# Optimization experiments

Hardware: AMD Instinct MI355X
Metric: run time of the kernel (lower is better)

## Reference

```python
import jax, jax.numpy as jnp
import numpy as np

B = 16384      # samples
NN = 11        # causal-graph nodes per sample (adult)
D = 4          # per-node raw feature dim (node_dim_max)
F = 32         # dim_input_enc = h_dim_list_enc[0]
EDIM = 4       # edge_dim
NI = 3         # number of intervention features

_BASE_EDGES = np.array([[0,3],[0,4],[1,3],[1,5],[2,5],[0,6],[3,6],[4,7],[5,7],
                        [6,8],[7,8],[2,9],[8,9],[3,10],[6,10],[9,10],[1,10]], dtype=np.int64)


def setup_inputs() -> dict:
    key = jax.random.key(0)
    ks = jax.random.split(key, 14)
    # batched edge index: replicate the 17-edge DAG per sample with node offsets
    off = (np.arange(B) * NN)[:, None]                      # [B,1]
    src = (_BASE_EDGES[:, 0][None, :] + off).reshape(-1).astype(np.int32)  # [E]
    dst = (_BASE_EDGES[:, 1][None, :] + off).reshape(-1).astype(np.int32)
    E = src.shape[0]
    g = lambda k, shp, s: jax.random.normal(k, shp, dtype=jnp.float32) * s
    return {
        'x_input':  g(ks[0], (B, NN * D), 1.0),
        'edge_attr': g(ks[1], (E, EDIM), 1.0),
        'W_emb':   g(ks[2], (NN, D, F), 1.0 / np.sqrt(D)),
        'b_emb':   jnp.zeros((NN, F), jnp.float32),
        'W_pre1':  g(ks[3], (NI, 2 * F + EDIM, F), 1.0 / np.sqrt(2 * F + EDIM)),
        'b_pre1':  jnp.zeros((NI, F), jnp.float32),
        'W_post1': g(ks[4], (NI, 12 * F, F), 1.0 / np.sqrt(12 * F)),
        'b_post1': jnp.zeros((NI, F), jnp.float32),
        'W_pre2':  g(ks[5], (NI, 2 * F + EDIM, F), 1.0 / np.sqrt(2 * F + EDIM)),
        'b_pre2':  jnp.zeros((NI, F), jnp.float32),
        'W_post2': g(ks[6], (NI, 12 * F, 1), 1.0 / np.sqrt(12 * F)),
        'b_post2': jnp.zeros((NI, 1), jnp.float32),
        'W_fc':    g(ks[7], (NI, NN, 1), 1.0 / np.sqrt(NN)),
        'b_fc':    jnp.zeros((NI, 1), jnp.float32),
        'edge_src': jnp.asarray(src),
        'edge_dst': jnp.asarray(dst),
    }


def _pna_conv(h, src, dst, e, Wpre, bpre, Wpost, bpost, cnt_c, mask, amp, att, N):
    # message: pre-MLP over [h_dst, h_src, edge_attr]
    m = jax.nn.relu(jnp.concatenate([h[dst], h[src], e], axis=1) @ Wpre + bpre)  # [E,F]
    s = jax.ops.segment_sum(m, dst, num_segments=N)
    mean = s / cnt_c[:, None]
    mean_sq = jax.ops.segment_sum(m * m, dst, num_segments=N) / cnt_c[:, None]
    std = jnp.sqrt(jax.nn.relu(mean_sq - mean * mean) + 1e-5)
    mn = jnp.where(mask[:, None], jax.ops.segment_min(m, dst, num_segments=N), 0.0)
    mx = jnp.where(mask[:, None], jax.ops.segment_max(m, dst, num_segments=N), 0.0)
    agg = jnp.concatenate([mean, mn, mx, std], axis=1)                 # [N,4F]
    scaled = jnp.concatenate([agg, agg * amp[:, None], agg * att[:, None]], axis=1)  # [N,12F]
    return scaled @ Wpost + bpost


def reference(x_input, edge_attr, W_emb, b_emb,
              W_pre1, b_pre1, W_post1, b_post1,
              W_pre2, b_pre2, W_post2, b_post2,
              W_fc, b_fc, edge_src, edge_dst):
    N = B * NN
    # encoder embeddings: per-node linear + relu (shared across interventions)
    X = x_input.reshape(B, NN, D)
    H = jax.nn.relu(jnp.einsum('bnd,ndf->bnf', X, W_emb) + b_emb).reshape(N, F)
    # degree stats for PNA scalers (in-degree)
    cnt = jax.ops.segment_sum(jnp.ones_like(edge_dst, dtype=jnp.float32), edge_dst, num_segments=N)
    mask = cnt > 0
    cnt_c = jnp.maximum(cnt, 1.0)
    logd = jnp.log1p(jnp.maximum(cnt, 1.0))
    avg_log = jnp.mean(logd)
    amp = logd / avg_log
    att = avg_log / logd
    outs = []
    for i in range(NI):
        h1 = jax.nn.relu(_pna_conv(H, edge_src, edge_dst, edge_attr,
                                   W_pre1[i], b_pre1[i], W_post1[i], b_post1[i],
                                   cnt_c, mask, amp, att, N))
        h2 = _pna_conv(h1, edge_src, edge_dst, edge_attr,
                       W_pre2[i], b_pre2[i], W_post2[i], b_post2[i],
                       cnt_c, mask, amp, att, N)            # [N,1]
        p = jax.nn.sigmoid(h2)                               # get_prob=True
        pm = p.reshape(B, NN).mean(axis=0)                   # return_mean=True -> [11]
        outs.append(pm @ W_fc[i] + b_fc[i])                  # [1]
    # padded sum over interventions == concatenation when inter_features == intervention_features
    return jnp.concatenate(outs)[None, :]                    # [1, NI]
```

## Files before the change

kernel.cpp:

```cpp
#include <hip/hip_runtime.h>
#include <math.h>

#define B_TOT   16384
#define SB      5
#define TPB     512

#define SSTRIDE 1488
#define OFF_H   0
#define OFF_EA  396
#define OFF_H1  464
#define OFF_AGG 752
#define OFF_TD  752
#define OFF_TS  1040
#define OFF_A4  576
#define OFF_A10 608
#define WLDS    (SB * SSTRIDE)

#define LW_B4   0
#define LW_H1C  32
#define LW_V1C1 64
#define LW_V10  160
#define LW_V4   288
#define LW_C42  320
#define LW_TSC  324
#define LW_BP1  356
#define LW_EA1  388
#define LW_EA2  516
#define LW_WC1  644
#define LTAB    3716

#define OFF_PACC (WLDS + LTAB)
#define LDS_FLOATS (WLDS + LTAB + 16)
#define AVG_LOG 0.9976091242438673f

#define G_WC1  0
#define G_W10  3072
#define G_W4   7168
#define G_SM   8192
#define WTAB   8548
#define WS_TAB 64

__constant__ int C_ESRC[17] = {0,0,1,1,2,0,3,4,5,6,7,2,8,3,6,9,1};
__constant__ int C1EA[6] = {0,3,5,7,9,11};
__constant__ int C1EB[6] = {2,4,6,8,10,12};
__constant__ int C1N[6]  = {3,5,6,7,8,9};

#define FMA16(a, wb, u) do { \
    float4 w0_ = *(const float4*)(wb); \
    float4 w1_ = *(const float4*)((wb) + 32); \
    float4 w2_ = *(const float4*)((wb) + 64); \
    float4 w3_ = *(const float4*)((wb) + 96); \
    u.x = fmaf(a.x, w0_.x, u.x); u.y = fmaf(a.x, w0_.y, u.y); u.z = fmaf(a.x, w0_.z, u.z); u.w = fmaf(a.x, w0_.w, u.w); \
    u.x = fmaf(a.y, w1_.x, u.x); u.y = fmaf(a.y, w1_.y, u.y); u.z = fmaf(a.y, w1_.z, u.z); u.w = fmaf(a.y, w1_.w, u.w); \
    u.x = fmaf(a.z, w2_.x, u.x); u.y = fmaf(a.z, w2_.y, u.y); u.z = fmaf(a.z, w2_.z, u.z); u.w = fmaf(a.z, w2_.w, u.w); \
    u.x = fmaf(a.w, w3_.x, u.x); u.y = fmaf(a.w, w3_.y, u.y); u.z = fmaf(a.w, w3_.z, u.z); u.w = fmaf(a.w, w3_.w, u.w); \
} while (0)

#define MSG(e_, m_) do { \
    const float4 ev_ = *(const float4*)(S + OFF_EA + (e_) * 4); \
    const float4 ts_ = *(const float4*)(S + OFF_TS + C_ESRC[(e_)] * 36 + f); \
    m_.x = base.x + ts_.x; m_.y = base.y + ts_.y; m_.z = base.z + ts_.z; m_.w = base.w + ts_.w; \
    m_.x = fmaf(ev_.x, w0.x, m_.x); m_.y = fmaf(ev_.x, w0.y, m_.y); m_.z = fmaf(ev_.x, w0.z, m_.z); m_.w = fmaf(ev_.x, w0.w, m_.w); \
    m_.x = fmaf(ev_.y, w1.x, m_.x); m_.y = fmaf(ev_.y, w1.y, m_.y); m_.z = fmaf(ev_.y, w1.z, m_.z); m_.w = fmaf(ev_.y, w1.w, m_.w); \
    m_.x = fmaf(ev_.z, w2.x, m_.x); m_.y = fmaf(ev_.z, w2.y, m_.y); m_.z = fmaf(ev_.z, w2.z, m_.z); m_.w = fmaf(ev_.z, w2.w, m_.w); \
    m_.x = fmaf(ev_.w, w3.x, m_.x); m_.y = fmaf(ev_.w, w3.y, m_.y); m_.z = fmaf(ev_.w, w3.z, m_.z); m_.w = fmaf(ev_.w, w3.w, m_.w); \
    m_.x = fmaxf(m_.x, 0.f); m_.y = fmaxf(m_.y, 0.f); m_.z = fmaxf(m_.z, 0.f); m_.w = fmaxf(m_.w, 0.f); \
} while (0)

static __device__ __forceinline__ float coef3(const float* __restrict__ W1, int r, int fcol, float amp, float att)
{
    return W1[r * 32 + fcol] + amp * W1[(128 + r) * 32 + fcol] + att * W1[(256 + r) * 32 + fcol];
}
static __device__ __forceinline__ float coef3s(const float* __restrict__ W2, int r, float amp, float att)
{
    return W2[r] + amp * W2[128 + r] + att * W2[256 + r];
}

extern "C" __global__ void pna_fold(const float* __restrict__ W_post1, const float* __restrict__ b_post1,
                                    const float* __restrict__ W_post2, const float* __restrict__ b_post2,
                                    const float* __restrict__ W_pre2,  float* __restrict__ ws)
{
    const int t0 = blockIdx.x * blockDim.x + threadIdx.x;
    const int NT = gridDim.x * blockDim.x;
    const float l1 = log1pf(1.f), l2 = log1pf(2.f), l4 = log1pf(4.f);
    const float amp1 = l1 / AVG_LOG, att1 = AVG_LOG / l1;
    const float amp2 = l2 / AVG_LOG, att2 = AVG_LOG / l2;
    const float amp4 = l4 / AVG_LOG, att4 = AVG_LOG / l4;
    const float SIG0 = 0.0031622776601683794f;

    for (int idx = t0; idx < 3 * WTAB; idx += NT) {
        const int i = idx / WTAB, off = idx % WTAB;
        const float* W1 = W_post1 + i * 384 * 32;
        const float* W2 = W_post2 + i * 384;
        float val = 0.f;
        if (off < 3072) {
            const int j = off >> 5, fcol = off & 31, sub = j >> 5, jj = j & 31;
            if (sub == 0)      val = coef3(W1, jj, fcol, amp2, att2) + 2.f * coef3(W1, 64 + jj, fcol, amp2, att2);
            else if (sub == 1) val = coef3(W1, 32 + jj, fcol, amp2, att2) - coef3(W1, 64 + jj, fcol, amp2, att2);
            else               val = coef3(W1, 96 + jj, fcol, amp2, att2);
        } else if (off < 7168) {
            const int rr = off - 3072;
            val = coef3(W1, rr >> 5, rr & 31, amp4, att4);
        } else if (off < 8192) {
            const int rr = off - 7168, jj = rr >> 5, fcol = rr & 31;
            val = coef3(W1, jj, fcol, amp1, att1) + coef3(W1, 32 + jj, fcol, amp1, att1)
                + coef3(W1, 64 + jj, fcol, amp1, att1);
        } else if (off < 8224) {
            const int fcol = off - 8192;
            float ssum = 0.f;
            for (int jj = 0; jj < 32; ++jj) ssum += coef3(W1, 96 + jj, fcol, amp1, att1);
            val = b_post1[i * 32 + fcol] + SIG0 * ssum;
        } else if (off < 8256) {
            const int fcol = off - 8224;
            float ssum = 0.f;
            for (int jj = 0; jj < 32; ++jj) ssum += coef3(W1, 96 + jj, fcol, amp1, att1);
            val = fmaxf(b_post1[i * 32 + fcol] + SIG0 * ssum, 0.f);
        } else if (off < 8352) {
            const int j = off - 8256, sub = j >> 5, jj = j & 31;
            if (sub == 0)      val = coef3s(W2, jj, amp2, att2) + 2.f * coef3s(W2, 64 + jj, amp2, att2);
            else if (sub == 1) val = coef3s(W2, 32 + jj, amp2, att2) - coef3s(W2, 64 + jj, amp2, att2);
            else               val = coef3s(W2, 96 + jj, amp2, att2);
        } else if (off < 8480) {
            val = coef3s(W2, off - 8352, amp4, att4);
        } else if (off < 8512) {
            const int jj = off - 8480;
            val = coef3s(W2, jj, amp1, att1) + coef3s(W2, 32 + jj, amp1, att1) + coef3s(W2, 64 + jj, amp1, att1);
        } else if (off == 8512) {
            float ssum = 0.f;
            for (int jj = 0; jj < 32; ++jj) ssum += coef3s(W2, 96 + jj, amp1, att1);
            val = SIG0 * ssum;
        } else if (off >= 8516 && off < 8548) {
            const int fcol = off - 8516;
            const float* Wp2 = W_pre2 + i * 2176;
            float acc = 0.f;
            for (int k = 0; k < 32; ++k) {
                float ssum = 0.f;
                for (int jj = 0; jj < 32; ++jj) ssum += coef3(W1, 96 + jj, k, amp1, att1);
                const float h1c = fmaxf(b_post1[i * 32 + k] + SIG0 * ssum, 0.f);
                acc = fmaf(h1c, Wp2[(32 + k) * 32 + fcol], acc);
            }
            val = acc;
        }
        ws[WS_TAB + idx] = val;
    }
    if (t0 < 40) ws[t0] = 0.f;
    if (t0 >= 40 && t0 < 43) {
        const int i = t0 - 40;
        const float* W2 = W_post2 + i * 384;
        float ssum = 0.f;
        for (int jj = 0; jj < 32; ++jj) ssum += coef3s(W2, 96 + jj, amp1, att1);
        ws[40 + i] = 1.f / (1.f + expf(-(b_post2[i] + SIG0 * ssum)));
    }
}

template<int PASS>
static __device__ __forceinline__ void conv_T(float* lds, const float* wl, int nsamp, int w, int lane,
                                              const float* __restrict__ Wp,
                                              const float* __restrict__ bp)
{
    const int ty = w & 1;
    const int f0 = (w >> 1) * 8;
    int s, n, tasks;
    if (ty == 0)            { tasks = nsamp * 8;  s = lane >> 3;  n = 3 + (lane & 7); }
    else if (PASS == 0)     { tasks = nsamp * 10; s = lane / 10;  n = lane % 10; }
    else                    { tasks = nsamp * 7;  s = lane / 7;   n = 3 + lane % 7; }
    const bool act = lane < tasks;
    if (!act) { s = 0; n = 3; }
    const float* Hrow = lds + s * SSTRIDE
        + (PASS == 0 ? (OFF_H + n * 36) : (OFF_H1 + (n - 3) * 36));
    const float* wbase = Wp + ty * 32 * 32 + f0;
    float acc[8];
#pragma unroll
    for (int f = 0; f < 8; f++) acc[f] = ty ? 0.f : bp[f0 + f];
#pragma unroll
    for (int kq = 0; kq < 8; kq++) {
        float4 a = *(const float4*)(Hrow + kq * 4);
#pragma unroll
        for (int kk = 0; kk < 4; kk++) {
            float av = (kk == 0) ? a.x : (kk == 1) ? a.y : (kk == 2) ? a.z : a.w;
            const float* wr = wbase + (kq * 4 + kk) * 32;
#pragma unroll
            for (int f = 0; f < 8; f++) acc[f] = fmaf(av, wr[f], acc[f]);
        }
    }
    float* T = lds + s * SSTRIDE + (ty ? (OFF_TS + n * 36) : (OFF_TD + (n - 3) * 36)) + f0;
    if (act) {
        *(float4*)(T + 0) = make_float4(acc[0], acc[1], acc[2], acc[3]);
        *(float4*)(T + 4) = make_float4(acc[4], acc[5], acc[6], acc[7]);
    }
    if (PASS == 1 && ty == 1) {
        if (lane < nsamp * 3) {
            const int cs = lane / 3, cn = lane % 3;
            float* Tc = lds + cs * SSTRIDE + OFF_TS + cn * 36 + f0;
            *(float4*)(Tc)     = *(const float4*)(wl + LW_TSC + f0);
            *(float4*)(Tc + 4) = *(const float4*)(wl + LW_TSC + f0 + 4);
        }
    }
}

template<int CONV2>
static __device__ __forceinline__ void fused_conv(float* lds, const float* wl, int nsamp,
                                                  int w, int lane, float b2, float* pacc)
{
    const bool act = lane < nsamp * 8;
    const int l = act ? lane : 0;
    const int s = l >> 3, q = l & 7, f = q * 4;
    float* S = lds + s * SSTRIDE;
    const float* WE = wl + (CONV2 ? LW_EA2 : LW_EA1) + f;
    const float4 w0 = *(const float4*)(WE);
    const float4 w1 = *(const float4*)(WE + 32);
    const float4 w2 = *(const float4*)(WE + 64);
    const float4 w3 = *(const float4*)(WE + 96);

    float4 r0 = make_float4(0.f,0.f,0.f,0.f), r1 = r0, r2 = r0, r3 = r0;
    float u = 0.f;

    if (w < 6) {
        float4 base = *(const float4*)(S + OFF_TD + (C1N[w] - 3) * 36 + f);
        float4 ma, mb;
        MSG(C1EA[w], ma);
        MSG(C1EB[w], mb);
        r0.x = (ma.x + mb.x) * 0.5f; r0.y = (ma.y + mb.y) * 0.5f;
        r0.z = (ma.z + mb.z) * 0.5f; r0.w = (ma.w + mb.w) * 0.5f;
        r1.x = fminf(ma.x, mb.x); r1.y = fminf(ma.y, mb.y);
        r1.z = fminf(ma.z, mb.z); r1.w = fminf(ma.w, mb.w);
        float4 msq;
        msq.x = fmaf(mb.x, mb.x, ma.x * ma.x) * 0.5f;
        msq.y = fmaf(mb.y, mb.y, ma.y * ma.y) * 0.5f;
        msq.z = fmaf(mb.z, mb.z, ma.z * ma.z) * 0.5f;
        msq.w = fmaf(mb.w, mb.w, ma.w * ma.w) * 0.5f;
        r2.x = sqrtf(fmaxf(msq.x - r0.x * r0.x, 0.f) + 1e-5f);
        r2.y = sqrtf(fmaxf(msq.y - r0.y * r0.y, 0.f) + 1e-5f);
        r2.z = sqrtf(fmaxf(msq.z - r0.z * r0.z, 0.f) + 1e-5f);
        r2.w = sqrtf(fmaxf(msq.w - r0.w * r0.w, 0.f) + 1e-5f);
        if (CONV2) {
            const float* V = wl + LW_V1C1 + f;
            const float4 v0 = *(const float4*)(V);
            const float4 v1 = *(const float4*)(V + 32);
            const float4 v2 = *(const float4*)(V + 64);
            u = fmaf(r0.x, v0.x, fmaf(r0.y, v0.y, fmaf(r0.z, v0.z, r0.w * v0.w)));
            u = fmaf(r1.x, v1.x, fmaf(r1.y, v1.y, fmaf(r1.z, v1.z, fmaf(r1.w, v1.w, u))));
            u = fmaf(r2.x, v2.x, fmaf(r2.y, v2.y, fmaf(r2.z, v2.z, fmaf(r2.w, v2.w, u))));
        }
    } else if (w == 6) {
        float4 base = *(const float4*)(S + OFF_TD + 1 * 36 + f);
        float4 m;
        MSG(1, m);
        r0 = m;
        if (CONV2) {
            const float4 v0 = *(const float4*)(wl + LW_V4 + f);
            u = fmaf(m.x, v0.x, fmaf(m.y, v0.y, fmaf(m.z, v0.z, m.w * v0.w)));
        }
    } else {
        float4 base = *(const float4*)(S + OFF_TD + 7 * 36 + f);
        float4 sum = make_float4(0.f,0.f,0.f,0.f), sq = sum;
        float4 mn = make_float4(1e30f,1e30f,1e30f,1e30f);
        float4 mx = make_float4(-1e30f,-1e30f,-1e30f,-1e30f);
#pragma unroll
        for (int e = 13; e <= 16; ++e) {
            float4 m;
            MSG(e, m);
            sum.x += m.x; sum.y += m.y; sum.z += m.z; sum.w += m.w;
            sq.x = fmaf(m.x, m.x, sq.x); sq.y = fmaf(m.y, m.y, sq.y);
            sq.z = fmaf(m.z, m.z, sq.z); sq.w = fmaf(m.w, m.w, sq.w);
            mn.x = fminf(mn.x, m.x); mn.y = fminf(mn.y, m.y); mn.z = fminf(mn.z, m.z); mn.w = fminf(mn.w, m.w);
            mx.x = fmaxf(mx.x, m.x); mx.y = fmaxf(mx.y, m.y); mx.z = fmaxf(mx.z, m.z); mx.w = fmaxf(mx.w, m.w);
        }
        r0.x = sum.x * 0.25f; r0.y = sum.y * 0.25f; r0.z = sum.z * 0.25f; r0.w = sum.w * 0.25f;
        r1 = mn; r2 = mx;
        float4 msq = make_float4(sq.x * 0.25f, sq.y * 0.25f, sq.z * 0.25f, sq.w * 0.25f);
        r3.x = sqrtf(fmaxf(msq.x - r0.x * r0.x, 0.f) + 1e-5f);
        r3.y = sqrtf(fmaxf(msq.y - r0.y * r0.y, 0.f) + 1e-5f);
        r3.z = sqrtf(fmaxf(msq.z - r0.z * r0.z, 0.f) + 1e-5f);
        r3.w = sqrtf(fmaxf(msq.w - r0.w * r0.w, 0.f) + 1e-5f);
        if (CONV2) {
            const float* V = wl + LW_V10 + f;
            const float4 v0 = *(const float4*)(V);
            const float4 v1 = *(const float4*)(V + 32);
            const float4 v2 = *(const float4*)(V + 64);
            const float4 v3 = *(const float4*)(V + 96);
            u = fmaf(r0.x, v0.x, fmaf(r0.y, v0.y, fmaf(r0.z, v0.z, r0.w * v0.w)));
            u = fmaf(r1.x, v1.x, fmaf(r1.y, v1.y, fmaf(r1.z, v1.z, fmaf(r1.w, v1.w, u))));
            u = fmaf(r2.x, v2.x, fmaf(r2.y, v2.y, fmaf(r2.z, v2.z, fmaf(r2.w, v2.w, u))));
            u = fmaf(r3.x, v3.x, fmaf(r3.y, v3.y, fmaf(r3.z, v3.z, fmaf(r3.w, v3.w, u))));
        }
    }

    if (!CONV2) {
        __syncthreads();
        if (act) {
            if (w < 6) {
                float* A = S + OFF_AGG + w * 96;
                *(float4*)(A + f) = r0; *(float4*)(A + 32 + f) = r1; *(float4*)(A + 64 + f) = r2;
            } else if (w == 6) {
                *(float4*)(S + OFF_AGG + OFF_A4 + f) = r0;
            } else {
                float* A = S + OFF_AGG + OFF_A10;
                *(float4*)(A + f) = r0; *(float4*)(A + 32 + f) = r1;
                *(float4*)(A + 64 + f) = r2; *(float4*)(A + 96 + f) = r3;
            }
        }
    } else {
        u += __shfl_xor(u, 1);
        u += __shfl_xor(u, 2);
        u += __shfl_xor(u, 4);
        if (act && q == 0) {
            const float extra = (w == 6) ? wl[LW_C42] : 0.f;
            const int node = (w < 6) ? C1N[w] : (w == 6 ? 4 : 10);
            const float p = 1.f / (1.f + expf(-(u + b2 + extra)));
            atomicAdd(pacc + node, p);
        }
    }
}

static __device__ __forceinline__ void post1_new(float* lds, const float* wl, int nsamp, int w, int lane,
                                                 const float* __restrict__ tabg)
{
    const bool act = lane < nsamp * 8;
    const int l = act ? lane : 0;
    const int s = l >> 3, q = l & 7;
    if (w < 6) {
        const float* A = lds + s * SSTRIDE + OFF_AGG + w * 96;
        const float* W = wl + LW_WC1 + q * 4;
        float4 u = make_float4(0.f,0.f,0.f,0.f);
#pragma unroll 1
        for (int jq = 0; jq < 24; ++jq) {
            float4 a = *(const float4*)(A + jq * 4);
            FMA16(a, W + jq * 128, u);
        }
        if (act) {
            const float4 b = *(const float4*)(wl + LW_BP1 + q * 4);
            float4 o;
            o.x = fmaxf(u.x + b.x, 0.f); o.y = fmaxf(u.y + b.y, 0.f);
            o.z = fmaxf(u.z + b.z, 0.f); o.w = fmaxf(u.w + b.w, 0.f);
            *(float4*)(lds + s * SSTRIDE + OFF_H1 + (C1N[w] - 3) * 36 + q * 4) = o;
        }
    } else if (w == 7) {
        const float* A = lds + s * SSTRIDE + OFF_AGG + OFF_A10;
        const float* W = tabg + G_W10 + q * 4;
        float4 u = make_float4(0.f,0.f,0.f,0.f);
#pragma unroll 2
        for (int jq = 0; jq < 32; ++jq) {
            float4 a = *(const float4*)(A + jq * 4);
            FMA16(a, W + jq * 128, u);
        }
        if (act) {
            const float4 b = *(const float4*)(wl + LW_BP1 + q * 4);
            float4 o;
            o.x = fmaxf(u.x + b.x, 0.f); o.y = fmaxf(u.y + b.y, 0.f);
            o.z = fmaxf(u.z + b.z, 0.f); o.w = fmaxf(u.w + b.w, 0.f);
            *(float4*)(lds + s * SSTRIDE + OFF_H1 + 7 * 36 + q * 4) = o;
        }
    } else {
        const float* A = lds + s * SSTRIDE + OFF_AGG + OFF_A4;
        const float* W = tabg + G_W4 + q * 4;
        float4 u = make_float4(0.f,0.f,0.f,0.f);
#pragma unroll 2
        for (int jq = 0; jq < 8; ++jq) {
            float4 a = *(const float4*)(A + jq * 4);
            FMA16(a, W + jq * 128, u);
        }
        if (act) {
            const float4 b = *(const float4*)(wl + LW_B4 + q * 4);
            float4 o;
            o.x = fmaxf(u.x + b.x, 0.f); o.y = fmaxf(u.y + b.y, 0.f);
            o.z = fmaxf(u.z + b.z, 0.f); o.w = fmaxf(u.w + b.w, 0.f);
            *(float4*)(lds + s * SSTRIDE + OFF_H1 + 1 * 36 + q * 4) = o;
        }
    }
}

extern "C" __global__ void __launch_bounds__(TPB, 4)
pna_main(const float* __restrict__ x_input, const float* __restrict__ edge_attr,
         const float* __restrict__ W_emb,  const float* __restrict__ b_emb,
         const float* __restrict__ W_pre1, const float* __restrict__ b_pre1,
         const float* __restrict__ b_post1,
         const float* __restrict__ W_pre2, const float* __restrict__ b_pre2,
         const float* __restrict__ b_post2,
         const float* __restrict__ wstab,  float* __restrict__ gacc)
{
    extern __shared__ float lds[];
    const int tid = threadIdx.x;
    const int w = __builtin_amdgcn_readfirstlane(tid >> 6);
    const int lane = tid & 63;
    const int s0 = blockIdx.x * SB;
    const int nsamp = min(SB, B_TOT - s0);
    float* wl = lds + WLDS;
    float* pacc = lds + OFF_PACC;

    if (tid < 16) pacc[tid] = 0.f;

    for (int t = tid; t < nsamp * 68; t += TPB)
        lds[(t / 68) * SSTRIDE + OFF_EA + (t % 68)] = edge_attr[(size_t)s0 * 68 + t];

    for (int t = tid; t < nsamp * 352; t += TPB) {
        const int s = t / 352, r = t % 352, n = r >> 5, f = r & 31;
        const float* Xs = x_input + (size_t)(s0 + s) * 44 + n * 4;
        const float* We = W_emb + (n * 4) * 32 + f;
        float v = b_emb[n * 32 + f];
        v = fmaf(Xs[0], We[0],  v);
        v = fmaf(Xs[1], We[32], v);
        v = fmaf(Xs[2], We[64], v);
        v = fmaf(Xs[3], We[96], v);
        lds[s * SSTRIDE + OFF_H + n * 36 + f] = fmaxf(v, 0.f);
    }
    __syncthreads();

    for (int i = 0; i < 3; i++) {
        const float* tab = wstab + i * WTAB;
        for (int t = tid; t < 768; t += TPB)
            ((float4*)(wl + LW_WC1))[t] = ((const float4*)(tab + G_WC1))[t];
        if (tid < 89)       ((float4*)wl)[tid] = ((const float4*)(tab + G_SM))[tid];
        else if (tid < 97)  ((float4*)(wl + LW_BP1))[tid - 89] = ((const float4*)(b_post1 + i * 32))[tid - 89];
        else if (tid < 129) ((float4*)(wl + LW_EA1))[tid - 97] = ((const float4*)(W_pre1 + i * 2176 + 2048))[tid - 97];
        else if (tid < 161) ((float4*)(wl + LW_EA2))[tid - 129] = ((const float4*)(W_pre2 + i * 2176 + 2048))[tid - 129];

        conv_T<0>(lds, wl, nsamp, w, lane, W_pre1 + i * 2176, b_pre1 + i * 32);
        __syncthreads();
        fused_conv<0>(lds, wl, nsamp, w, lane, 0.f, pacc);
        __syncthreads();
        post1_new(lds, wl, nsamp, w, lane, tab);
        __syncthreads();
        conv_T<1>(lds, wl, nsamp, w, lane, W_pre2 + i * 2176, b_pre2 + i * 32);
        __syncthreads();
        fused_conv<1>(lds, wl, nsamp, w, lane, b_post2[i], pacc);
        __syncthreads();
        if (tid < 11) {
            atomicAdd(gacc + i * 11 + tid, pacc[tid]);
            pacc[tid] = 0.f;
        }
    }
}

extern "C" __global__ void pna_final(const float* __restrict__ ws,
                                     const float* __restrict__ W_fc,
                                     const float* __restrict__ b_fc,
                                     float* __restrict__ out)
{
    const int i = threadIdx.x;
    if (i < 3) {
        float acc = 0.f;
        for (int n = 0; n < 11; n++)
            acc = fmaf(ws[i * 11 + n] * (1.f / 16384.f), W_fc[i * 11 + n], acc);
        const float pc = ws[40 + i];
        const float wsum = W_fc[i * 11 + 0] + W_fc[i * 11 + 1] + W_fc[i * 11 + 2];
        out[i] = acc + pc * wsum + b_fc[i];
    }
}

extern "C" void kernel_launch(void* const* d_in, const int* in_sizes, int n_in,
                              void* d_out, int out_size, void* d_ws, size_t ws_size,
                              hipStream_t stream)
{
    (void)in_sizes; (void)n_in; (void)out_size; (void)ws_size;
    const float* x_input   = (const float*)d_in[0];
    const float* edge_attr = (const float*)d_in[1];
    const float* W_emb     = (const float*)d_in[2];
    const float* b_emb     = (const float*)d_in[3];
    const float* W_pre1    = (const float*)d_in[4];
    const float* b_pre1    = (const float*)d_in[5];
    const float* W_post1   = (const float*)d_in[6];
    const float* b_post1   = (const float*)d_in[7];
    const float* W_pre2    = (const float*)d_in[8];
    const float* b_pre2    = (const float*)d_in[9];
    const float* W_post2   = (const float*)d_in[10];
    const float* b_post2   = (const float*)d_in[11];
    const float* W_fc      = (const float*)d_in[12];
    const float* b_fc      = (const float*)d_in[13];
    float* ws  = (float*)d_ws;
    float* out = (float*)d_out;

    hipLaunchKernelGGL(pna_fold, dim3(64), dim3(512), 0, stream,
                       W_post1, b_post1, W_post2, b_post2, W_pre2, ws);
    const int grid = (B_TOT + SB - 1) / SB;
    const size_t shmem = (size_t)LDS_FLOATS * sizeof(float);
    hipLaunchKernelGGL(pna_main, dim3(grid), dim3(TPB), shmem, stream,
                       x_input, edge_attr, W_emb, b_emb,
                       W_pre1, b_pre1, b_post1,
                       W_pre2, b_pre2, b_post2,
                       ws + WS_TAB, ws);
    hipLaunchKernelGGL(pna_final, dim3(1), dim3(64), 0, stream, ws, W_fc, b_fc, out);
}
```

Measured before the change: 354.9 us.

## Fuse conv1 post-MLP into aggregation via wave shuffles, drop LDS staging

```diff
diff --git a/kernel.cpp b/kernel.cpp
--- a/kernel.cpp
+++ b/kernel.cpp
@@ -2,18 +2,15 @@
 #include <math.h>
 
 #define B_TOT   16384
-#define SB      5
+#define SB      6
 #define TPB     512
 
-#define SSTRIDE 1488
+#define SSTRIDE 1420
 #define OFF_H   0
 #define OFF_EA  396
 #define OFF_H1  464
-#define OFF_AGG 752
 #define OFF_TD  752
 #define OFF_TS  1040
-#define OFF_A4  576
-#define OFF_A10 608
 #define WLDS    (SB * SSTRIDE)
 
 #define LW_B4   0
@@ -54,6 +51,11 @@
     u.x = fmaf(a.y, w1_.x, u.x); u.y = fmaf(a.y, w1_.y, u.y); u.z = fmaf(a.y, w1_.z, u.z); u.w = fmaf(a.y, w1_.w, u.w); \
     u.x = fmaf(a.z, w2_.x, u.x); u.y = fmaf(a.z, w2_.y, u.y); u.z = fmaf(a.z, w2_.z, u.z); u.w = fmaf(a.z, w2_.w, u.w); \
     u.x = fmaf(a.w, w3_.x, u.x); u.y = fmaf(a.w, w3_.y, u.y); u.z = fmaf(a.w, w3_.z, u.z); u.w = fmaf(a.w, w3_.w, u.w); \
+} while (0)
+
+#define SHFL4(rb_, src_, a_) do { \
+    a_.x = __shfl(rb_.x, src_); a_.y = __shfl(rb_.y, src_); \
+    a_.z = __shfl(rb_.z, src_); a_.w = __shfl(rb_.w, src_); \
 } while (0)
 
 #define MSG(e_, m_) do { \
@@ -200,7 +202,8 @@
 
 template<int CONV2>
 static __device__ __forceinline__ void fused_conv(float* lds, const float* wl, int nsamp,
-                                                  int w, int lane, float b2, float* pacc)
+                                                  int w, int lane, float b2, float* pacc,
+                                                  const float* __restrict__ tabg)
 {
     const bool act = lane < nsamp * 8;
     const int l = act ? lane : 0;
@@ -214,6 +217,8 @@
 
     float4 r0 = make_float4(0.f,0.f,0.f,0.f), r1 = r0, r2 = r0, r3 = r0;
     float u = 0.f;
+    const int gbase = lane & 56;
+    const int qc = lane & 7;
 
     if (w < 6) {
         float4 base = *(const float4*)(S + OFF_TD + (C1N[w] - 3) * 36 + f);
@@ -241,6 +246,26 @@
             u = fmaf(r0.x, v0.x, fmaf(r0.y, v0.y, fmaf(r0.z, v0.z, r0.w * v0.w)));
             u = fmaf(r1.x, v1.x, fmaf(r1.y, v1.y, fmaf(r1.z, v1.z, fmaf(r1.w, v1.w, u))));
             u = fmaf(r2.x, v2.x, fmaf(r2.y, v2.y, fmaf(r2.z, v2.z, fmaf(r2.w, v2.w, u))));
+        } else {
+            float4 u4 = make_float4(0.f,0.f,0.f,0.f);
+            const float* W = wl + LW_WC1 + qc * 4;
+#pragma unroll 1
+            for (int b = 0; b < 3; ++b) {
+                const float4 rb = (b == 0) ? r0 : (b == 1) ? r1 : r2;
+#pragma unroll
+                for (int qq = 0; qq < 8; ++qq) {
+                    float4 a4;
+                    SHFL4(rb, gbase + qq, a4);
+                    FMA16(a4, W + (b * 8 + qq) * 128, u4);
+                }
+            }
+            if (act) {
+                const float4 b4 = *(const float4*)(wl + LW_BP1 + f);
+                float4 o;
+                o.x = fmaxf(u4.x + b4.x, 0.f); o.y = fmaxf(u4.y + b4.y, 0.f);
+                o.z = fmaxf(u4.z + b4.z, 0.f); o.w = fmaxf(u4.w + b4.w, 0.f);
+                *(float4*)(lds + s * SSTRIDE + OFF_H1 + (C1N[w] - 3) * 36 + f) = o;
+            }
         }
     } else if (w == 6) {
         float4 base = *(const float4*)(S + OFF_TD + 1 * 36 + f);
@@ -250,6 +275,22 @@
         if (CONV2) {
             const float4 v0 = *(const float4*)(wl + LW_V4 + f);
             u = fmaf(m.x, v0.x, fmaf(m.y, v0.y, fmaf(m.z, v0.z, m.w * v0.w)));
+        } else {
+            float4 u4 = make_float4(0.f,0.f,0.f,0.f);
+            const float* W = tabg + G_W4 + qc * 4;
+#pragma unroll 2
+            for (int qq = 0; qq < 8; ++qq) {
+                float4 a4;
+                SHFL4(r0, gbase + qq, a4);
+                FMA16(a4, W + qq * 128, u4);
+            }
+            if (act) {
+                const float4 b4 = *(const float4*)(wl + LW_B4 + f);
+                float4 o;
+                o.x = fmaxf(u4.x + b4.x, 0.f); o.y = fmaxf(u4.y + b4.y, 0.f);
+                o.z = fmaxf(u4.z + b4.z, 0.f); o.w = fmaxf(u4.w + b4.w, 0.f);
+                *(float4*)(lds + s * SSTRIDE + OFF_H1 + 1 * 36 + f) = o;
+            }
         }
     } else {
         float4 base = *(const float4*)(S + OFF_TD + 7 * 36 + f);
@@ -283,24 +324,30 @@
             u = fmaf(r1.x, v1.x, fmaf(r1.y, v1.y, fmaf(r1.z, v1.z, fmaf(r1.w, v1.w, u))));
             u = fmaf(r2.x, v2.x, fmaf(r2.y, v2.y, fmaf(r2.z, v2.z, fmaf(r2.w, v2.w, u))));
             u = fmaf(r3.x, v3.x, fmaf(r3.y, v3.y, fmaf(r3.z, v3.z, fmaf(r3.w, v3.w, u))));
-        }
-    }
-
-    if (!CONV2) {
-        __syncthreads();
-        if (act) {
-            if (w < 6) {
-                float* A = S + OFF_AGG + w * 96;
-                *(float4*)(A + f) = r0; *(float4*)(A + 32 + f) = r1; *(float4*)(A + 64 + f) = r2;
-            } else if (w == 6) {
-                *(float4*)(S + OFF_AGG + OFF_A4 + f) = r0;
-            } else {
-                float* A = S + OFF_AGG + OFF_A10;
-                *(float4*)(A + f) = r0; *(float4*)(A + 32 + f) = r1;
-                *(float4*)(A + 64 + f) = r2; *(float4*)(A + 96 + f) = r3;
-            }
-        }
-    } else {
+        } else {
+            float4 u4 = make_float4(0.f,0.f,0.f,0.f);
+            const float* W = tabg + G_W10 + qc * 4;
+#pragma unroll 1
+            for (int b = 0; b < 4; ++b) {
+                const float4 rb = (b == 0) ? r0 : (b == 1) ? r1 : (b == 2) ? r2 : r3;
+#pragma unroll
+                for (int qq = 0; qq < 8; ++qq) {
+                    float4 a4;
+                    SHFL4(rb, gbase + qq, a4);
+                    FMA16(a4, W + (b * 8 + qq) * 128, u4);
+                }
+            }
+            if (act) {
+                const float4 b4 = *(const float4*)(wl + LW_BP1 + f);
+                float4 o;
+                o.x = fmaxf(u4.x + b4.x, 0.f); o.y = fmaxf(u4.y + b4.y, 0.f);
+                o.z = fmaxf(u4.z + b4.z, 0.f); o.w = fmaxf(u4.w + b4.w, 0.f);
+                *(float4*)(lds + s * SSTRIDE + OFF_H1 + 7 * 36 + f) = o;
+            }
+        }
+    }
+
+    if (CONV2) {
         u += __shfl_xor(u, 1);
         u += __shfl_xor(u, 2);
         u += __shfl_xor(u, 4);
@@ -309,63 +356,6 @@
             const int node = (w < 6) ? C1N[w] : (w == 6 ? 4 : 10);
             const float p = 1.f / (1.f + expf(-(u + b2 + extra)));
             atomicAdd(pacc + node, p);
-        }
-    }
-}
-
-static __device__ __forceinline__ void post1_new(float* lds, const float* wl, int nsamp, int w, int lane,
-                                                 const float* __restrict__ tabg)
-{
-    const bool act = lane < nsamp * 8;
-    const int l = act ? lane : 0;
-    const int s = l >> 3, q = l & 7;
-    if (w < 6) {
-        const float* A = lds + s * SSTRIDE + OFF_AGG + w * 96;
-        const float* W = wl + LW_WC1 + q * 4;
-        float4 u = make_float4(0.f,0.f,0.f,0.f);
-#pragma unroll 1
-        for (int jq = 0; jq < 24; ++jq) {
-            float4 a = *(const float4*)(A + jq * 4);
-            FMA16(a, W + jq * 128, u);
-        }
-        if (act) {
-            const float4 b = *(const float4*)(wl + LW_BP1 + q * 4);
-            float4 o;
-            o.x = fmaxf(u.x + b.x, 0.f); o.y = fmaxf(u.y + b.y, 0.f);
-            o.z = fmaxf(u.z + b.z, 0.f); o.w = fmaxf(u.w + b.w, 0.f);
-            *(float4*)(lds + s * SSTRIDE + OFF_H1 + (C1N[w] - 3) * 36 + q * 4) = o;
-        }
-    } else if (w == 7) {
-        const float* A = lds + s * SSTRIDE + OFF_AGG + OFF_A10;
-        const float* W = tabg + G_W10 + q * 4;
-        float4 u = make_float4(0.f,0.f,0.f,0.f);
-#pragma unroll 2
-        for (int jq = 0; jq < 32; ++jq) {
-            float4 a = *(const float4*)(A + jq * 4);
-            FMA16(a, W + jq * 128, u);
-        }
-        if (act) {
-            const float4 b = *(const float4*)(wl + LW_BP1 + q * 4);
-            float4 o;
-            o.x = fmaxf(u.x + b.x, 0.f); o.y = fmaxf(u.y + b.y, 0.f);
-            o.z = fmaxf(u.z + b.z, 0.f); o.w = fmaxf(u.w + b.w, 0.f);
-            *(float4*)(lds + s * SSTRIDE + OFF_H1 + 7 * 36 + q * 4) = o;
-        }
-    } else {
-        const float* A = lds + s * SSTRIDE + OFF_AGG + OFF_A4;
-        const float* W = tabg + G_W4 + q * 4;
-        float4 u = make_float4(0.f,0.f,0.f,0.f);
-#pragma unroll 2
-        for (int jq = 0; jq < 8; ++jq) {
-            float4 a = *(const float4*)(A + jq * 4);
-            FMA16(a, W + jq * 128, u);
-        }
-        if (act) {
-            const float4 b = *(const float4*)(wl + LW_B4 + q * 4);
-            float4 o;
-            o.x = fmaxf(u.x + b.x, 0.f); o.y = fmaxf(u.y + b.y, 0.f);
-            o.z = fmaxf(u.z + b.z, 0.f); o.w = fmaxf(u.w + b.w, 0.f);
-            *(float4*)(lds + s * SSTRIDE + OFF_H1 + 1 * 36 + q * 4) = o;
         }
     }
 }
@@ -417,13 +407,11 @@
 
         conv_T<0>(lds, wl, nsamp, w, lane, W_pre1 + i * 2176, b_pre1 + i * 32);
         __syncthreads();
-        fused_conv<0>(lds, wl, nsamp, w, lane, 0.f, pacc);
-        __syncthreads();
-        post1_new(lds, wl, nsamp, w, lane, tab);
+        fused_conv<0>(lds, wl, nsamp, w, lane, 0.f, pacc, tab);
         __syncthreads();
         conv_T<1>(lds, wl, nsamp, w, lane, W_pre2 + i * 2176, b_pre2 + i * 32);
         __syncthreads();
-        fused_conv<1>(lds, wl, nsamp, w, lane, b_post2[i], pacc);
+        fused_conv<1>(lds, wl, nsamp, w, lane, b_post2[i], pacc, tab);
         __syncthreads();
         if (tid < 11) {
             atomicAdd(gacc + i * 11 + tid, pacc[tid]);
```

Result: no change. 353.4 us (-0.4%).
